# Kernel tuning notes

Measured on AMD Instinct MI355X. Metric: run time of the kernel, lower is better.

## Reference

```python
import jax, jax.numpy as jnp
import numpy as np
from jax import lax

BS = 8  # block size
NF = 64  # num_feat

def _dct_mat(n=BS):
    k = np.arange(n)
    D = np.cos(np.pi * (2 * k[None, :] + 1) * k[:, None] / (2 * n)) * np.sqrt(2.0 / n)
    D[0] = np.sqrt(1.0 / n)
    return jnp.asarray(D, dtype=jnp.float32)  # orthonormal DCT-II basis [8,8]

D_DCT = _dct_mat()

def conv2d(x, w, b, stride=1, padding=0, dilation=1, groups=1):
    out = lax.conv_general_dilated(
        x, w, window_strides=(stride, stride),
        padding=[(padding, padding), (padding, padding)],
        rhs_dilation=(dilation, dilation),
        feature_group_count=groups,
        dimension_numbers=('NCHW', 'OIHW', 'NCHW'))
    return out + b[None, :, None, None]

def block_dct_idct(x, bs=BS):
    # fused per-8x8-block DDCT followed by IDDCT (orthonormal basis ->
    # mathematically identity, computed explicitly as in the original loop)
    B, C, H, W = x.shape
    xb = x.reshape(B, C, H // bs, bs, W // bs, bs)
    CB = jnp.einsum('ij,bchjwk,lk->bchiwl', D_DCT, xb, D_DCT)   # D X D^T
    out = jnp.einsum('ji,bchjwk,kl->bchiwl', D_DCT, CB, D_DCT)  # D^T Y D
    return out.reshape(B, C, H, W)

def setup_inputs() -> dict:
    key = jax.random.key(0)
    ks = jax.random.split(key, 16)
    s = 0.05
    inp = {
        'x': jax.random.normal(ks[0], (2, 72, 256, 256), dtype=jnp.float32),
        'conv_w': jax.random.normal(ks[1], (64, 72, 3, 3), dtype=jnp.float32) * s,
        'conv_b': jnp.zeros((64,), dtype=jnp.float32),
        # 7 distinct directional_dct_layer instances (branch 6 reuses layer 4's weights, as in the source)
        'ddct_w': jax.random.normal(ks[2], (7, 64, 64, 3, 3), dtype=jnp.float32) * s,
        'ddct_b': jnp.zeros((7, 64), dtype=jnp.float32),
        'dctc_w': jax.random.normal(ks[3], (7, 64, 1, 3, 3), dtype=jnp.float32) * s,  # groups=64 depthwise
        'dctc_b': jnp.zeros((7, 64), dtype=jnp.float32),
        'dw1_w': jax.random.normal(ks[4], (32, 72, 3, 3), dtype=jnp.float32) * s,
        'dw1_b': jnp.zeros((32,), dtype=jnp.float32),
        'dw3_w': jax.random.normal(ks[5], (512, 32, 1, 1), dtype=jnp.float32) * s,
        'dw3_b': jnp.zeros((512,), dtype=jnp.float32),
        'ar_w': jax.random.normal(ks[6], (72, 512, 3, 3), dtype=jnp.float32) * s,
        'ar_b': jnp.zeros((72,), dtype=jnp.float32),
    }
    return inp

def reference(x, conv_w, conv_b, ddct_w, ddct_b, dctc_w, dctc_b,
              dw1_w, dw1_b, dw3_w, dw3_b, ar_w, ar_b):
    B, _, H, W = x.shape
    feat = jax.nn.gelu(conv2d(x, conv_w, conv_b, padding=1), approximate=False)
    # branches use layers [0,1,3,4,5,6(->4),7,8]; branch 6 reuses conv_dct_4
    layer_idx = [0, 1, 2, 3, 4, 3, 5, 6]
    outs = []
    for li in layer_idx:
        y = jax.nn.gelu(conv2d(feat, ddct_w[li], ddct_b[li], padding=1), approximate=False) + feat
        y = conv2d(y, dctc_w[li], dctc_b[li], stride=8, padding=2, dilation=2, groups=NF)
        y = block_dct_idct(y)
        y = jax.image.resize(y, (B, NF, H, W), method='bilinear')  # align_corners=False
        outs.append(y)
    w = jax.nn.sigmoid(conv2d(jax.nn.relu(conv2d(x, dw1_w, dw1_b, padding=1)), dw3_w, dw3_b, padding=0))
    gated = jnp.concatenate([o * w[:, i * NF:(i + 1) * NF] for i, o in enumerate(outs)], axis=1)
    return conv2d(gated, ar_w, ar_b, padding=1)
```

## Files before the change

kernel.cpp:

```cpp
#include <hip/hip_runtime.h>
#include <hip/hip_bf16.h>

#define BB 2
#define HH 256
#define WW 256
#define HW (HH*WW)

typedef __attribute__((ext_vector_type(8))) short bf16x8;
typedef __attribute__((ext_vector_type(4))) float f32x4;

__device__ __forceinline__ float geluf(float x) {
    return 0.5f * x * (1.0f + erff(x * 0.7071067811865475f));
}

__device__ __forceinline__ ushort f2bf(float f) {
    __hip_bfloat16 h = __float2bfloat16(f);
    return *reinterpret_cast<ushort*>(&h);
}
__device__ __forceinline__ float bf2f(ushort u) {
    uint v = ((uint)u) << 16;
    return *reinterpret_cast<float*>(&v);
}

__device__ __forceinline__ int dec96(int i) {
    int q = i / 3, r = i - q * 3;
    return q * 8 + (r == 0 ? 0 : (r == 1 ? 2 : 6));
}

__global__ __launch_bounds__(256) void xpose_kernel(
    const float* __restrict__ x, ushort* __restrict__ xt)
{
    const int pix = blockIdx.x * 256 + threadIdx.x;
    const int b   = pix >> 16;
    const int rem = pix & 65535;

    uint w[48];
    const float* xb = x + (size_t)b * 72 * HW + rem;
    #pragma unroll
    for (int i = 0; i < 36; ++i) {
        const ushort lo = f2bf(xb[(size_t)(2 * i)     * HW]);
        const ushort hi = f2bf(xb[(size_t)(2 * i + 1) * HW]);
        w[i] = (uint)lo | ((uint)hi << 16);
    }
    #pragma unroll
    for (int i = 36; i < 48; ++i) w[i] = 0;

    uint* dst = reinterpret_cast<uint*>(xt + (size_t)pix * 96);
    #pragma unroll
    for (int k = 0; k < 12; ++k) {
        uint4 u = { w[4*k], w[4*k+1], w[4*k+2], w[4*k+3] };
        *reinterpret_cast<uint4*>(dst + 4 * k) = u;
    }
}

__global__ __launch_bounds__(256) void prepack_w1_kernel(
    const float* __restrict__ conv_w, const float* __restrict__ dw1_w,
    ushort* __restrict__ wpc1)
{
    const int idx = blockIdx.x * 256 + threadIdx.x;
    if (idx >= 9 * 3 * 6 * 64) return;
    const int lane = idx & 63;
    int rest = idx >> 6;
    const int mf = rest % 6; rest /= 6;
    const int cb = rest % 3;
    const int t  = rest / 3;
    const int co  = mf * 16 + (lane & 15);
    const int ci0 = cb * 32 + (lane >> 4) * 8;
    ushort* dst = wpc1 + (size_t)idx * 8;
    #pragma unroll
    for (int j = 0; j < 8; ++j) {
        const int ci = ci0 + j;
        float w = 0.0f;
        if (ci < 72)
            w = (co < 64) ? conv_w[((size_t)co * 72 + ci) * 9 + t]
                          : dw1_w[((size_t)(co - 64) * 72 + ci) * 9 + t];
        dst[j] = f2bf(w);
    }
}

__global__ __launch_bounds__(256) void conv1dw1_mfma_kernel(
    const ushort* __restrict__ xt, const ushort* __restrict__ wpc1,
    const float* __restrict__ conv_b, const float* __restrict__ dw1_b,
    ushort* __restrict__ fg, float* __restrict__ relu1)
{
    const int lane = threadIdx.x & 63;
    const int wave = threadIdx.x >> 6;
    const int l15  = lane & 15;
    const int lg   = lane >> 4;

    const int bid  = blockIdx.x;
    const int b    = bid >> 9;
    const int rest = bid & 511;
    const int y    = rest >> 1;
    const int x0   = (rest & 1) * 128 + wave * 32;

    f32x4 acc[6][2];
    #pragma unroll
    for (int mf = 0; mf < 6; ++mf)
        #pragma unroll
        for (int nf = 0; nf < 2; ++nf)
            acc[mf][nf] = (f32x4){0.f, 0.f, 0.f, 0.f};

    const bf16x8 zero8 = {};

    #pragma unroll 1
    for (int t = 0; t < 9; ++t) {
        const int dy = t / 3 - 1, dx = t % 3 - 1;
        const int yy = y + dy;
        if ((unsigned)yy >= (unsigned)HH) continue;

        const int xA = x0 + l15 + dx;
        const int xB = xA + 16;
        const bool va = (unsigned)xA < (unsigned)WW;
        const bool vb = (unsigned)xB < (unsigned)WW;
        const int xAc = min(max(xA, 0), WW - 1);
        const int xBc = min(xB, WW - 1);

        const ushort* rowbase = xt + ((size_t)(b * HH + yy) * WW) * 96;
        const ushort* pA = rowbase + (size_t)xAc * 96 + lg * 8;
        const ushort* pB = rowbase + (size_t)xBc * 96 + lg * 8;
        const ushort* wp = wpc1 + (size_t)(t * 3) * (6 * 512) + lane * 8;

        #pragma unroll
        for (int cb = 0; cb < 3; ++cb) {
            bf16x8 B0 = *reinterpret_cast<const bf16x8*>(pA + cb * 32);
            bf16x8 B1 = *reinterpret_cast<const bf16x8*>(pB + cb * 32);
            B0 = va ? B0 : zero8;
            B1 = vb ? B1 : zero8;
            const ushort* wpc = wp + (size_t)cb * (6 * 512);
            #pragma unroll
            for (int mf = 0; mf < 6; ++mf) {
                const bf16x8 A = *reinterpret_cast<const bf16x8*>(wpc + mf * 512);
                acc[mf][0] = __builtin_amdgcn_mfma_f32_16x16x32_bf16(A, B0, acc[mf][0], 0, 0, 0);
                acc[mf][1] = __builtin_amdgcn_mfma_f32_16x16x32_bf16(A, B1, acc[mf][1], 0, 0, 0);
            }
        }
    }

    #pragma unroll
    for (int nf = 0; nf < 2; ++nf) {
        const int xx = x0 + nf * 16 + l15;
        ushort* fgp = fg + ((size_t)(b * HH + y) * WW + xx) * 64;
        #pragma unroll
        for (int mf = 0; mf < 4; ++mf) {
            const int co = mf * 16 + lg * 4;
            ushort pk[4];
            #pragma unroll
            for (int r = 0; r < 4; ++r)
                pk[r] = f2bf(geluf(acc[mf][nf][r] + conv_b[co + r]));
            *reinterpret_cast<uint2*>(fgp + co) = *reinterpret_cast<uint2*>(pk);
        }
    }
    #pragma unroll
    for (int mf = 4; mf < 6; ++mf) {
        const int co = (mf - 4) * 16 + lg * 4;
        #pragma unroll
        for (int nf = 0; nf < 2; ++nf) {
            const int xx = x0 + nf * 16 + l15;
            float* op = relu1 + ((size_t)(b * 32 + co) * HH + y) * WW + xx;
            #pragma unroll
            for (int r = 0; r < 4; ++r)
                op[(size_t)r * HW] = fmaxf(acc[mf][nf][r] + dw1_b[co + r], 0.0f);
        }
    }
}

__global__ __launch_bounds__(256) void prepack_wb_kernel(
    const float* __restrict__ ddct_w, ushort* __restrict__ wpb)
{
    const int idx = blockIdx.x * 256 + threadIdx.x;
    if (idx >= 7 * 9 * 2 * 4 * 64) return;
    const int lane = idx & 63;
    int rest = idx >> 6;
    const int mf = rest & 3; rest >>= 2;
    const int cb = rest & 1; rest >>= 1;
    const int t  = rest % 9;
    const int li = rest / 9;
    const int co  = mf * 16 + (lane & 15);
    const int ci0 = cb * 32 + (lane >> 4) * 8;
    ushort* dst = wpb + (size_t)idx * 8;
    #pragma unroll
    for (int j = 0; j < 8; ++j)
        dst[j] = f2bf(ddct_w[(((size_t)li * 64 + co) * 64 + ci0 + j) * 9 + t]);
}

__global__ __launch_bounds__(256) void branch_mfma_kernel(
    const ushort* __restrict__ fg, const ushort* __restrict__ wpb,
    const float* __restrict__ ddct_b, float* __restrict__ ycomp)
{
    const int lane = threadIdx.x & 63;
    const int wave = threadIdx.x >> 6;
    const int l15  = lane & 15;
    const int lg   = lane >> 4;

    int bid = blockIdx.x;
    const int t72 = bid % 72; bid /= 72;
    const int b  = bid & 1;
    const int li = bid >> 1;
    const int widx = t72 * 4 + wave;
    const int r  = widx / 3;
    const int c0 = (widx - r * 3) * 32;
    const int R  = dec96(r);

    const int cA = c0 + l15, cB = cA + 16;
    const int CA = dec96(cA), CB2 = dec96(cB);

    f32x4 acc[4][2];
    #pragma unroll
    for (int mf = 0; mf < 4; ++mf)
        #pragma unroll
        for (int nf = 0; nf < 2; ++nf)
            acc[mf][nf] = (f32x4){0.f, 0.f, 0.f, 0.f};

    const bf16x8 zero8 = {};
    const ushort* fgb = fg + (size_t)b * HW * 64;

    #pragma unroll 1
    for (int t = 0; t < 9; ++t) {
        const int dy = t / 3 - 1, dx = t % 3 - 1;
        const int yy = R + dy;
        if ((unsigned)yy >= (unsigned)HH) continue;

        const int xA = CA + dx, xB = CB2 + dx;
        const bool va = (unsigned)xA < (unsigned)WW;
        const bool vb = (unsigned)xB < (unsigned)WW;
        const int xAc = min(max(xA, 0), WW - 1);
        const int xBc = min(max(xB, 0), WW - 1);

        const ushort* rowb = fgb + (size_t)yy * WW * 64;
        const ushort* pA = rowb + (size_t)xAc * 64 + lg * 8;
        const ushort* pB = rowb + (size_t)xBc * 64 + lg * 8;
        const ushort* wp = wpb + (size_t)((li * 9 + t) * 2) * (4 * 512) + lane * 8;

        #pragma unroll
        for (int cb = 0; cb < 2; ++cb) {
            bf16x8 B0 = *reinterpret_cast<const bf16x8*>(pA + cb * 32);
            bf16x8 B1 = *reinterpret_cast<const bf16x8*>(pB + cb * 32);
            B0 = va ? B0 : zero8;
            B1 = vb ? B1 : zero8;
            const ushort* wpc = wp + (size_t)cb * (4 * 512);
            #pragma unroll
            for (int mf = 0; mf < 4; ++mf) {
                const bf16x8 A = *reinterpret_cast<const bf16x8*>(wpc + mf * 512);
                acc[mf][0] = __builtin_amdgcn_mfma_f32_16x16x32_bf16(A, B0, acc[mf][0], 0, 0, 0);
                acc[mf][1] = __builtin_amdgcn_mfma_f32_16x16x32_bf16(A, B1, acc[mf][1], 0, 0, 0);
            }
        }
    }

    #pragma unroll
    for (int nf = 0; nf < 2; ++nf) {
        const int c = c0 + nf * 16 + l15;
        const int C = dec96(c);
        const ushort* res = fgb + ((size_t)R * WW + C) * 64;
        #pragma unroll
        for (int mf = 0; mf < 4; ++mf) {
            const int co = mf * 16 + lg * 4;
            ushort r4[4];
            *reinterpret_cast<uint2*>(r4) = *reinterpret_cast<const uint2*>(res + co);
            #pragma unroll
            for (int rr = 0; rr < 4; ++rr) {
                const float v = geluf(acc[mf][nf][rr] + ddct_b[li * 64 + co + rr]) + bf2f(r4[rr]);
                ycomp[((((size_t)li * BB + b) * 64 + co + rr) * 96 + r) * 96 + c] = v;
            }
        }
    }
}

__global__ __launch_bounds__(256) void dctc_kernel(
    const float* __restrict__ ycomp, const float* __restrict__ dctc_w,
    const float* __restrict__ dctc_b, float* __restrict__ s_all)
{
    const int idx = blockIdx.x * 256 + threadIdx.x;
    if (idx >= 7 * BB * 64 * 32 * 32) return;
    const int ow = idx & 31;
    const int oh = (idx >> 5) & 31;
    const int c  = (idx >> 10) & 63;
    const int b  = (idx >> 16) & (BB - 1);
    const int li = idx >> 17;

    const float* yc = ycomp + (((size_t)li * BB + b) * 64 + c) * (96 * 96);
    const float* w  = dctc_w + (li * 64 + c) * 9;
    float acc = dctc_b[li * 64 + c];
    #pragma unroll
    for (int ky = 0; ky < 3; ++ky) {
        const int cr = 3 * oh + ky - 1;
        if (cr < 0) continue;
        #pragma unroll
        for (int kx = 0; kx < 3; ++kx) {
            const int cc = 3 * ow + kx - 1;
            if (cc < 0) continue;
            acc = fmaf(yc[cr * 96 + cc], w[ky * 3 + kx], acc);
        }
    }
    s_all[idx] = acc;
}

__global__ __launch_bounds__(256) void prepack_w3_kernel(
    const float* __restrict__ dw3_w, float* __restrict__ dw3t)
{
    const int idx = blockIdx.x * 256 + threadIdx.x;
    if (idx >= 32 * 512) return;
    const int ch = idx & 511;
    const int k  = idx >> 9;
    dw3t[k * 512 + ch] = dw3_w[ch * 32 + k];
}

__global__ __launch_bounds__(256, 3) void gated_nhwc_kernel(
    const float* __restrict__ relu1, const float* __restrict__ dw3t,
    const float* __restrict__ dw3_b, const float* __restrict__ s_all,
    ushort* __restrict__ gt)
{
    __shared__ float sm[32][32];
    const int pix0 = blockIdx.x * 32;
    const int b  = pix0 >> 16;
    const int y  = (pix0 >> 8) & 255;
    const int x0 = pix0 & 255;

    {
        const int spx = threadIdx.x & 31;
        const int k0  = threadIdx.x >> 5;
        const float* rbase = relu1 + (size_t)b * 32 * HW + (size_t)y * WW + x0 + spx;
        #pragma unroll
        for (int i = 0; i < 4; ++i)
            sm[k0 + 8 * i][spx] = rbase[(size_t)(k0 + 8 * i) * HW];
    }
    __syncthreads();

    const int ch0 = threadIdx.x * 2;
    const int branch = ch0 >> 6;
    const int c0 = ch0 & 63;
    const int lmap[8] = {0, 1, 2, 3, 4, 3, 5, 6};
    const int li = lmap[branch];

    const float bb0 = dw3_b[ch0], bb1 = dw3_b[ch0 + 1];

    float2 wreg[32];
    #pragma unroll
    for (int k = 0; k < 32; ++k)
        wreg[k] = *reinterpret_cast<const float2*>(dw3t + k * 512 + ch0);

    float acc0[32], acc1[32];
    #pragma unroll
    for (int px = 0; px < 32; ++px) { acc0[px] = bb0; acc1[px] = bb1; }

    #pragma unroll
    for (int k = 0; k < 32; ++k) {
        const float w0k = wreg[k].x;
        const float w1k = wreg[k].y;
        const float4* row = reinterpret_cast<const float4*>(&sm[k][0]);
        #pragma unroll
        for (int q = 0; q < 8; ++q) {
            const float4 r4 = row[q];
            acc0[q*4+0] = fmaf(r4.x, w0k, acc0[q*4+0]);
            acc0[q*4+1] = fmaf(r4.y, w0k, acc0[q*4+1]);
            acc0[q*4+2] = fmaf(r4.z, w0k, acc0[q*4+2]);
            acc0[q*4+3] = fmaf(r4.w, w0k, acc0[q*4+3]);
            acc1[q*4+0] = fmaf(r4.x, w1k, acc1[q*4+0]);
            acc1[q*4+1] = fmaf(r4.y, w1k, acc1[q*4+1]);
            acc1[q*4+2] = fmaf(r4.z, w1k, acc1[q*4+2]);
            acc1[q*4+3] = fmaf(r4.w, w1k, acc1[q*4+3]);
        }
    }

    const float* sp0 = s_all + (((size_t)li * BB + b) * 64 + c0) * 1024;
    const float* sp1 = sp0 + 1024;

    const float sy = (y + 0.5f) * 0.125f - 0.5f;
    const float fy0f = floorf(sy);
    const float fy = sy - fy0f;
    int y0 = (int)fy0f;
    const int y1 = min(y0 + 1, 31);
    y0 = max(y0, 0);

    float n0[6], n1[6];
    const int xb = (x0 >> 3) - 1;
    #pragma unroll
    for (int jj = 0; jj < 6; ++jj) {
        const int xn = min(max(xb + jj, 0), 31);
        const float a00 = sp0[y0 * 32 + xn], a01 = sp0[y1 * 32 + xn];
        const float a10 = sp1[y0 * 32 + xn], a11 = sp1[y1 * 32 + xn];
        n0[jj] = a00 + fy * (a01 - a00);
        n1[jj] = a10 + fy * (a11 - a10);
    }

    ushort* gbase = gt + (size_t)pix0 * 512 + ch0;
    #pragma unroll
    for (int px = 0; px < 32; ++px) {
        const int   j  = (px + 4) >> 3;
        const float fx = (float)((px + 4) & 7) * 0.125f + 0.0625f;
        const float va = n0[j] + fx * (n0[j + 1] - n0[j]);
        const float vb = n1[j] + fx * (n1[j + 1] - n1[j]);
        const float g0 = 1.0f / (1.0f + exp2f(-1.4426950408889634f * acc0[px]));
        const float g1 = 1.0f / (1.0f + exp2f(-1.4426950408889634f * acc1[px]));
        const uint pack = (uint)f2bf(va * g0) | ((uint)f2bf(vb * g1) << 16);
        *reinterpret_cast<uint*>(gbase + (size_t)px * 512) = pack;
    }
}

__global__ __launch_bounds__(256) void prepack_w_kernel(
    const float* __restrict__ ar_w, ushort* __restrict__ wpack)
{
    const int idx = blockIdx.x * 256 + threadIdx.x;
    if (idx >= 16 * 9 * 5 * 64) return;
    const int lane = idx & 63;
    int rest = idx >> 6;
    const int mf = rest % 5; rest /= 5;
    const int t  = rest % 9;
    const int cb = rest / 9;
    const int co  = mf * 16 + (lane & 15);
    const int ci0 = cb * 32 + (lane >> 4) * 8;
    ushort* dst = wpack + (size_t)idx * 8;
    #pragma unroll
    for (int j = 0; j < 8; ++j) {
        const float w = (co < 72) ? ar_w[((size_t)co * 512 + ci0 + j) * 9 + t] : 0.0f;
        dst[j] = f2bf(w);
    }
}

#define WPK_CHUNK (9 * 5 * 512)

__global__ __launch_bounds__(256, 2) void conv_ar_mfma_kernel(
    const ushort* __restrict__ gt, const ushort* __restrict__ wpack,
    const float* __restrict__ ar_b, float* __restrict__ out)
{
    __shared__ ushort smw[WPK_CHUNK];
    const int tid  = threadIdx.x;
    const int lane = tid & 63;
    const int wave = tid >> 6;
    const int l15  = lane & 15;
    const int lg   = lane >> 4;

    const int lb = (blockIdx.x & 7) * 64 + (blockIdx.x >> 3);
    const int b  = lb >> 8;
    const int y  = lb & 255;
    const int x0 = wave * 64;

    f32x4 acc[5][4];
    #pragma unroll
    for (int mf = 0; mf < 5; ++mf)
        #pragma unroll
        for (int nf = 0; nf < 4; ++nf)
            acc[mf][nf] = (f32x4){0.f, 0.f, 0.f, 0.f};

    const ushort* rowp[3];
    bool rowok[3];
    #pragma unroll
    for (int dy = 0; dy < 3; ++dy) {
        const int yy = y + dy - 1;
        rowok[dy] = (unsigned)yy < (unsigned)HH;
        rowp[dy]  = gt + ((size_t)(b * HH + (rowok[dy] ? yy : 0)) * WW) * 512;
    }
    int  offx[3][4];
    bool vx[3][4];
    #pragma unroll
    for (int dx = 0; dx < 3; ++dx) {
        #pragma unroll
        for (int nf = 0; nf < 4; ++nf) {
            const int xx = x0 + nf * 16 + l15 + dx - 1;
            vx[dx][nf]   = (unsigned)xx < (unsigned)WW;
            offx[dx][nf] = min(max(xx, 0), WW - 1) * 512 + lg * 8;
        }
    }

    const bf16x8 zero8 = {};

    #pragma unroll 1
    for (int cb = 0; cb < 16; ++cb) {
        __syncthreads();
        {
            const uint4* src = reinterpret_cast<const uint4*>(wpack + (size_t)cb * WPK_CHUNK);
            uint4* dst = reinterpret_cast<uint4*>(smw);
            #pragma unroll
            for (int i = 0; i < 12; ++i) {
                const int e = i * 256 + tid;
                if (e < 2880) dst[e] = src[e];
            }
        }
        __syncthreads();

        const int cbo = cb * 32;
        #pragma unroll
        for (int t = 0; t < 9; ++t) {
            const int dy = t / 3, dx = t % 3;
            if (!rowok[dy]) continue;
            bf16x8 Bv[4];
            #pragma unroll
            for (int nf = 0; nf < 4; ++nf) {
                bf16x8 v = *reinterpret_cast<const bf16x8*>(rowp[dy] + offx[dx][nf] + cbo);
                Bv[nf] = vx[dx][nf] ? v : zero8;
            }
            const ushort* wl = smw + (t * 5) * 512 + lane * 8;
            #pragma unroll
            for (int mf = 0; mf < 5; ++mf) {
                const bf16x8 A = *reinterpret_cast<const bf16x8*>(wl + mf * 512);
                #pragma unroll
                for (int nf = 0; nf < 4; ++nf)
                    acc[mf][nf] = __builtin_amdgcn_mfma_f32_16x16x32_bf16(A, Bv[nf], acc[mf][nf], 0, 0, 0);
            }
        }
    }

    #pragma unroll
    for (int mf = 0; mf < 5; ++mf) {
        const int co = mf * 16 + lg * 4;
        if (co >= 72) continue;
        #pragma unroll
        for (int nf = 0; nf < 4; ++nf) {
            const int x = x0 + nf * 16 + l15;
            float* op = out + (((size_t)(b * 72 + co) * HH + y) * WW) + x;
            #pragma unroll
            for (int r = 0; r < 4; ++r)
                op[(size_t)r * HW] = acc[mf][nf][r] + ar_b[co + r];
        }
    }
}

extern "C" void kernel_launch(void* const* d_in, const int* in_sizes, int n_in,
                              void* d_out, int out_size, void* d_ws, size_t ws_size,
                              hipStream_t stream) {
    const float* x      = (const float*)d_in[0];
    const float* conv_w = (const float*)d_in[1];
    const float* conv_b = (const float*)d_in[2];
    const float* ddct_w = (const float*)d_in[3];
    const float* ddct_b = (const float*)d_in[4];
    const float* dctc_w = (const float*)d_in[5];
    const float* dctc_b = (const float*)d_in[6];
    const float* dw1_w  = (const float*)d_in[7];
    const float* dw1_b  = (const float*)d_in[8];
    const float* dw3_w  = (const float*)d_in[9];
    const float* dw3_b  = (const float*)d_in[10];
    const float* ar_w   = (const float*)d_in[11];
    const float* ar_b   = (const float*)d_in[12];
    float* out = (float*)d_out;

    float* ws = (float*)d_ws;
    ushort* gated_t = (ushort*)ws;
    ushort* fg    = (ushort*)ws;
    float* ycomp  = ws + 4194304;
    float* s_all  = ws + 33554432;
    float* relu1  = ws + 34471936;
    ushort* wpack = (ushort*)(ws + 38666240);
    ushort* wpb   = (ushort*)(ws + 38850560);
    ushort* wpc1  = (ushort*)(ws + 38979584);
    ushort* xt    = (ushort*)(ws + 39021056);
    float* dw3t   = ws + 45312512;

    prepack_w_kernel<<<dim3(180), dim3(256), 0, stream>>>(ar_w, wpack);
    prepack_wb_kernel<<<dim3(126), dim3(256), 0, stream>>>(ddct_w, wpb);
    prepack_w1_kernel<<<dim3(41), dim3(256), 0, stream>>>(conv_w, dw1_w, wpc1);
    prepack_w3_kernel<<<dim3(64), dim3(256), 0, stream>>>(dw3_w, dw3t);
    xpose_kernel<<<dim3(BB * HW / 256), dim3(256), 0, stream>>>(x, xt);

    conv1dw1_mfma_kernel<<<dim3(BB * HH * 2), dim3(256), 0, stream>>>(
        xt, wpc1, conv_b, dw1_b, fg, relu1);

    branch_mfma_kernel<<<dim3(7 * BB * 72), dim3(256), 0, stream>>>(
        fg, wpb, ddct_b, ycomp);

    dctc_kernel<<<dim3((7 * BB * 64 * 32 * 32) / 256), dim3(256), 0, stream>>>(
        ycomp, dctc_w, dctc_b, s_all);

    gated_nhwc_kernel<<<dim3(BB * HW / 32), dim3(256), 0, stream>>>(
        relu1, dw3t, dw3_b, s_all, gated_t);

    conv_ar_mfma_kernel<<<dim3(BB * HH), dim3(256), 0, stream>>>(
        gated_t, wpack, ar_b, out);
}
```

Before: 402.6 us.

## Pad gated tensor with zero halo and reorder conv loop tap-outer

The gated NHWC buffer is stored with a one-pixel zero border (258x258), filled by a new halo_zero kernel, so the final 3x3 conv no longer needs per-load bounds checks or selects. The conv loop becomes tap-outer, channel-block-inner, staging only the first four output-row fragments per tap in shared memory and reading the fifth (rows 64-79, mostly padding) straight from global. Workspace offsets shift to fit the larger buffer. The cost is an extra small launch, slightly more memory, and a global-memory weight load inside the inner loop.

```diff
diff --git a/kernel.cpp b/kernel.cpp
--- a/kernel.cpp
+++ b/kernel.cpp
@@ -5,6 +5,8 @@
 #define HH 256
 #define WW 256
 #define HW (HH*WW)
+#define GP 258
+#define GPP (GP*GP)
 
 typedef __attribute__((ext_vector_type(8))) short bf16x8;
 typedef __attribute__((ext_vector_type(4))) float f32x4;
@@ -306,6 +308,31 @@
     dw3t[k * 512 + ch] = dw3_w[ch * 32 + k];
 }
 
+__global__ __launch_bounds__(256) void halo_zero_kernel(ushort* __restrict__ gt)
+{
+    const int PB = 2 * GP * 64 + 2 * 256 * 64;
+    const int i = blockIdx.x * 256 + threadIdx.x;
+    if (i >= BB * PB) return;
+    const int b = i / PB;
+    int r = i - b * PB;
+    size_t px;
+    int c4;
+    if (r < 2 * GP * 64) {
+        const int rr = r / (GP * 64);
+        int rem = r - rr * (GP * 64);
+        const int xp = rem / 64; c4 = rem % 64;
+        px = (size_t)(rr ? GP - 1 : 0) * GP + xp;
+    } else {
+        r -= 2 * GP * 64;
+        const int side = r / (256 * 64);
+        int rem = r - side * (256 * 64);
+        const int yp = 1 + rem / 64; c4 = rem % 64;
+        px = (size_t)yp * GP + (side ? GP - 1 : 0);
+    }
+    const uint4 z = {0u, 0u, 0u, 0u};
+    *reinterpret_cast<uint4*>(gt + ((size_t)b * GPP + px) * 512 + c4 * 8) = z;
+}
+
 __global__ __launch_bounds__(256, 3) void gated_nhwc_kernel(
     const float* __restrict__ relu1, const float* __restrict__ dw3t,
     const float* __restrict__ dw3_b, const float* __restrict__ s_all,
@@ -384,7 +411,7 @@
         n1[jj] = a10 + fy * (a11 - a10);
     }
 
-    ushort* gbase = gt + (size_t)pix0 * 512 + ch0;
+    ushort* gbase = gt + (((size_t)b * GPP) + (size_t)(y + 1) * GP + (x0 + 1)) * 512 + ch0;
     #pragma unroll
     for (int px = 0; px < 32; ++px) {
         const int   j  = (px + 4) >> 3;
@@ -399,18 +426,21 @@
 }
 
 __global__ __launch_bounds__(256) void prepack_w_kernel(
-    const float* __restrict__ ar_w, ushort* __restrict__ wpack)
+    const float* __restrict__ ar_w, ushort* __restrict__ wpA,
+    ushort* __restrict__ wpB)
 {
     const int idx = blockIdx.x * 256 + threadIdx.x;
-    if (idx >= 16 * 9 * 5 * 64) return;
+    if (idx >= 9 * 16 * 5 * 64) return;
     const int lane = idx & 63;
     int rest = idx >> 6;
     const int mf = rest % 5; rest /= 5;
-    const int t  = rest % 9;
-    const int cb = rest / 9;
+    const int cb = rest % 16;
+    const int t  = rest / 16;
     const int co  = mf * 16 + (lane & 15);
     const int ci0 = cb * 32 + (lane >> 4) * 8;
-    ushort* dst = wpack + (size_t)idx * 8;
+    ushort* dst = (mf < 4)
+        ? wpA + ((((size_t)(t * 16 + cb) * 4 + mf) * 64 + lane) * 8)
+        : wpB + (((size_t)(t * 16 + cb) * 64 + lane) * 8);
     #pragma unroll
     for (int j = 0; j < 8; ++j) {
         const float w = (co < 72) ? ar_w[((size_t)co * 512 + ci0 + j) * 9 + t] : 0.0f;
@@ -418,13 +448,14 @@
     }
 }
 
-#define WPK_CHUNK (9 * 5 * 512)
+#define WPA_TAP (16 * 4 * 512)
 
 __global__ __launch_bounds__(256, 2) void conv_ar_mfma_kernel(
-    const ushort* __restrict__ gt, const ushort* __restrict__ wpack,
-    const float* __restrict__ ar_b, float* __restrict__ out)
-{
-    __shared__ ushort smw[WPK_CHUNK];
+    const ushort* __restrict__ gt, const ushort* __restrict__ wpA,
+    const ushort* __restrict__ wpB, const float* __restrict__ ar_b,
+    float* __restrict__ out)
+{
+    __shared__ ushort smw[WPA_TAP];
     const int tid  = threadIdx.x;
     const int lane = tid & 63;
     const int wave = tid >> 6;
@@ -443,61 +474,44 @@
         for (int nf = 0; nf < 4; ++nf)
             acc[mf][nf] = (f32x4){0.f, 0.f, 0.f, 0.f};
 
-    const ushort* rowp[3];
-    bool rowok[3];
-    #pragma unroll
-    for (int dy = 0; dy < 3; ++dy) {
-        const int yy = y + dy - 1;
-        rowok[dy] = (unsigned)yy < (unsigned)HH;
-        rowp[dy]  = gt + ((size_t)(b * HH + (rowok[dy] ? yy : 0)) * WW) * 512;
-    }
-    int  offx[3][4];
-    bool vx[3][4];
-    #pragma unroll
-    for (int dx = 0; dx < 3; ++dx) {
-        #pragma unroll
-        for (int nf = 0; nf < 4; ++nf) {
-            const int xx = x0 + nf * 16 + l15 + dx - 1;
-            vx[dx][nf]   = (unsigned)xx < (unsigned)WW;
-            offx[dx][nf] = min(max(xx, 0), WW - 1) * 512 + lg * 8;
-        }
-    }
-
-    const bf16x8 zero8 = {};
-
     #pragma unroll 1
-    for (int cb = 0; cb < 16; ++cb) {
+    for (int t = 0; t < 9; ++t) {
+        const int dy = t / 3, dx = t % 3;
+
         __syncthreads();
         {
-            const uint4* src = reinterpret_cast<const uint4*>(wpack + (size_t)cb * WPK_CHUNK);
+            const uint4* src = reinterpret_cast<const uint4*>(wpA + (size_t)t * WPA_TAP);
             uint4* dst = reinterpret_cast<uint4*>(smw);
             #pragma unroll
-            for (int i = 0; i < 12; ++i) {
-                const int e = i * 256 + tid;
-                if (e < 2880) dst[e] = src[e];
-            }
+            for (int i = 0; i < 16; ++i)
+                dst[i * 256 + tid] = src[i * 256 + tid];
         }
         __syncthreads();
 
-        const int cbo = cb * 32;
-        #pragma unroll
-        for (int t = 0; t < 9; ++t) {
-            const int dy = t / 3, dx = t % 3;
-            if (!rowok[dy]) continue;
+        const ushort* rowP = gt + ((size_t)b * GPP + (size_t)(y + dy) * GP) * 512;
+        int off[4];
+        #pragma unroll
+        for (int nf = 0; nf < 4; ++nf)
+            off[nf] = (x0 + nf * 16 + l15 + dx) * 512 + lg * 8;
+        const ushort* wB_t = wpB + (size_t)t * (16 * 512) + lane * 8;
+
+        #pragma unroll 4
+        for (int cb = 0; cb < 16; ++cb) {
             bf16x8 Bv[4];
             #pragma unroll
-            for (int nf = 0; nf < 4; ++nf) {
-                bf16x8 v = *reinterpret_cast<const bf16x8*>(rowp[dy] + offx[dx][nf] + cbo);
-                Bv[nf] = vx[dx][nf] ? v : zero8;
-            }
-            const ushort* wl = smw + (t * 5) * 512 + lane * 8;
-            #pragma unroll
-            for (int mf = 0; mf < 5; ++mf) {
-                const bf16x8 A = *reinterpret_cast<const bf16x8*>(wl + mf * 512);
+            for (int nf = 0; nf < 4; ++nf)
+                Bv[nf] = *reinterpret_cast<const bf16x8*>(rowP + off[nf] + cb * 32);
+            const bf16x8 A4 = *reinterpret_cast<const bf16x8*>(wB_t + (size_t)cb * 512);
+            #pragma unroll
+            for (int mf = 0; mf < 4; ++mf) {
+                const bf16x8 A = *reinterpret_cast<const bf16x8*>(smw + (cb * 4 + mf) * 512 + lane * 8);
                 #pragma unroll
                 for (int nf = 0; nf < 4; ++nf)
                     acc[mf][nf] = __builtin_amdgcn_mfma_f32_16x16x32_bf16(A, Bv[nf], acc[mf][nf], 0, 0, 0);
             }
+            #pragma unroll
+            for (int nf = 0; nf < 4; ++nf)
+                acc[4][nf] = __builtin_amdgcn_mfma_f32_16x16x32_bf16(A4, Bv[nf], acc[4][nf], 0, 0, 0);
         }
     }
 
@@ -538,15 +552,16 @@
     ushort* gated_t = (ushort*)ws;
     ushort* fg    = (ushort*)ws;
     float* ycomp  = ws + 4194304;
-    float* s_all  = ws + 33554432;
-    float* relu1  = ws + 34471936;
-    ushort* wpack = (ushort*)(ws + 38666240);
-    ushort* wpb   = (ushort*)(ws + 38850560);
-    ushort* wpc1  = (ushort*)(ws + 38979584);
-    ushort* xt    = (ushort*)(ws + 39021056);
-    float* dw3t   = ws + 45312512;
-
-    prepack_w_kernel<<<dim3(180), dim3(256), 0, stream>>>(ar_w, wpack);
+    float* s_all  = ws + 34080768;
+    float* relu1  = ws + 34998272;
+    ushort* wpA   = (ushort*)(ws + 39192576);
+    ushort* wpB   = (ushort*)(ws + 39340032);
+    ushort* wpb   = (ushort*)(ws + 39376896);
+    ushort* wpc1  = (ushort*)(ws + 39505920);
+    ushort* xt    = (ushort*)(ws + 39547392);
+    float* dw3t   = ws + 45838848;
+
+    prepack_w_kernel<<<dim3(180), dim3(256), 0, stream>>>(ar_w, wpA, wpB);
     prepack_wb_kernel<<<dim3(126), dim3(256), 0, stream>>>(ddct_w, wpb);
     prepack_w1_kernel<<<dim3(41), dim3(256), 0, stream>>>(conv_w, dw1_w, wpc1);
     prepack_w3_kernel<<<dim3(64), dim3(256), 0, stream>>>(dw3_w, dw3t);
@@ -561,9 +576,11 @@
     dctc_kernel<<<dim3((7 * BB * 64 * 32 * 32) / 256), dim3(256), 0, stream>>>(
         ycomp, dctc_w, dctc_b, s_all);
 
+    halo_zero_kernel<<<dim3(514), dim3(256), 0, stream>>>(gated_t);
+
     gated_nhwc_kernel<<<dim3(BB * HW / 32), dim3(256), 0, stream>>>(
         relu1, dw3t, dw3_b, s_all, gated_t);
 
     conv_ar_mfma_kernel<<<dim3(BB * HH), dim3(256), 0, stream>>>(
-        gated_t, wpack, ar_b, out);
-}
+        gated_t, wpA, wpB, ar_b, out);
+}
```

Result: slower. 423.2 us (+5.1%).
